# Optimization experiments

Measured on AMD Instinct MI355X. Metric: run time of the kernel, lower is better.

Reference implementation:

```python
import jax, jax.numpy as jnp
import numpy as np

B, S, T, D, H, HD = 1, 2048, 256, 3072, 24, 128
FF = 4 * D
EPS_LN = 1e-6
EPS_RMS = 1e-6


def _layernorm(x):
    m = jnp.mean(x, axis=-1, keepdims=True)
    v = jnp.mean(jnp.square(x - m), axis=-1, keepdims=True)
    return (x - m) * jax.lax.rsqrt(v + EPS_LN)


def _rmsnorm(x, w):
    return x * jax.lax.rsqrt(jnp.mean(jnp.square(x), axis=-1, keepdims=True) + EPS_RMS) * w


def _rope_interleaved(x, cos, sin):
    # x: [B,S,H,HD], cos/sin: [S,HD//2]; non-neox (interleaved) style
    x1 = x[..., 0::2]
    x2 = x[..., 1::2]
    c = cos[None, :, None, :]
    s = sin[None, :, None, :]
    o1 = x1 * c - x2 * s
    o2 = x2 * c + x1 * s
    return jnp.stack([o1, o2], axis=-1).reshape(x.shape)


def setup_inputs() -> dict:
    key = jax.random.key(0)
    ks = jax.random.split(key, 12)

    def n(k, shape, scale):
        return jax.random.normal(k, shape, dtype=jnp.float32) * scale

    # real RoPE tables
    pos = np.arange(S, dtype=np.float64)
    inv_freq = 1.0 / (10000.0 ** (np.arange(0, HD, 2, dtype=np.float64) / HD))
    ang = np.outer(pos, inv_freq)  # [S, HD//2]

    return {
        "img": n(ks[0], (B, S, D), 1.0),
        "vec": n(ks[1], (B, D), 1.0),
        "cos": jnp.asarray(np.cos(ang), jnp.float32),
        "sin": jnp.asarray(np.sin(ang), jnp.float32),
        "k_txt": n(ks[2], (B, T, H, HD), 1.0),
        "v_txt": n(ks[3], (B, T, H, HD), 1.0),
        "mod_w": n(ks[4], (D, 6 * D), 0.02),
        "mod_b": jnp.zeros((6 * D,), jnp.float32),
        "qkv_w": n(ks[5], (D, 3 * D), 0.02),
        "qkv_b": jnp.zeros((3 * D,), jnp.float32),
        "qn_w": jnp.ones((HD,), jnp.float32),
        "kn_w": jnp.ones((HD,), jnp.float32),
        "proj_w": n(ks[6], (D, D), 0.02),
        "proj_b": jnp.zeros((D,), jnp.float32),
        "mlp_w1": n(ks[7], (D, FF), 0.02),
        "mlp_b1": jnp.zeros((FF,), jnp.float32),
        "mlp_w2": n(ks[8], (FF, D), 0.02),
        "mlp_b2": jnp.zeros((D,), jnp.float32),
    }


def reference(img, vec, cos, sin, k_txt, v_txt, mod_w, mod_b, qkv_w, qkv_b,
              qn_w, kn_w, proj_w, proj_b, mlp_w1, mlp_b1, mlp_w2, mlp_b2):
    # modulation: silu(vec) -> linear -> 6 chunks, each [B,1,D]
    mod = jax.nn.silu(vec) @ mod_w + mod_b
    (a_shift, a_scale, a_gate, m_shift, m_scale, m_gate) = [
        m[:, None, :] for m in jnp.split(mod, 6, axis=-1)
    ]

    # LayerNorm (no affine) + scale/shift modulate
    x = _layernorm(img) * (1.0 + a_scale) + a_shift

    qkv = (x @ qkv_w + qkv_b).reshape(B, S, 3, H, HD)
    q, k, v = qkv[:, :, 0], qkv[:, :, 1], qkv[:, :, 2]
    q = _rmsnorm(q, qn_w)
    k = _rmsnorm(k, kn_w)
    q = _rope_interleaved(q, cos, sin)
    k = _rope_interleaved(k, cos, sin)

    # concat text KV cache (no RoPE on text tokens)
    k_all = jnp.concatenate([k, k_txt], axis=1)  # [B,S+T,H,HD]
    v_all = jnp.concatenate([v, v_txt], axis=1)

    scale = 1.0 / jnp.sqrt(jnp.asarray(HD, jnp.float32))
    scores = jnp.einsum('bqhd,bkhd->bhqk', q, k_all) * scale
    probs = jax.nn.softmax(scores, axis=-1)
    attn = jnp.einsum('bhqk,bkhd->bqhd', probs, v_all).reshape(B, S, D)

    attn_out = attn @ proj_w + proj_b

    # ScaleResidualLayerNormScaleShift
    residual = img + a_gate * attn_out
    mlp_in = _layernorm(residual) * (1.0 + m_scale) + m_shift

    mlp_out = jax.nn.gelu(mlp_in @ mlp_w1 + mlp_b1, approximate=True) @ mlp_w2 + mlp_b2
    return residual + m_gate * mlp_out
```

## Files before the change

kernel.cpp:

```cpp
#include <hip/hip_runtime.h>

typedef short short8 __attribute__((ext_vector_type(8)));
typedef float f32x4 __attribute__((ext_vector_type(4)));

#define DEV static __device__ __forceinline__

DEV unsigned short f2bf(float f) {
  union { float f; unsigned u; } v; v.f = f;
  unsigned u = v.u;
  unsigned r = u + 0x7fffu + ((u >> 16) & 1u);
  return (unsigned short)(r >> 16);
}
DEV float bf2f(unsigned short b) {
  union { unsigned u; float f; } v; v.u = ((unsigned)b) << 16;
  return v.f;
}
DEV void load_lds16(const void* g, void* l) {
  __builtin_amdgcn_global_load_lds(
      (const __attribute__((address_space(1))) unsigned int*)g,
      (__attribute__((address_space(3))) unsigned int*)l, 16, 0, 0);
}
DEV int swz(int L) { return L ^ ((L >> 3) & 0x30); }

__global__ __launch_bounds__(256) void zero_mod(const float* __restrict__ b, float* __restrict__ out) {
  int j = blockIdx.x * 256 + threadIdx.x;
  out[j] = b[j];
}

__global__ __launch_bounds__(256) void mod_gemv(const float* __restrict__ vec,
                                                const float* __restrict__ W,
                                                float* __restrict__ out) {
  __shared__ float sv[192];
  int tid = threadIdx.x;
  int kb = blockIdx.y * 192;
  if (tid < 192) {
    float x = vec[kb + tid];
    sv[tid] = x / (1.f + __expf(-x));
  }
  __syncthreads();
  int j = blockIdx.x * 256 + tid;
  float a0 = 0, a1 = 0, a2 = 0, a3 = 0;
  for (int i = 0; i < 192; i += 4) {
    a0 += sv[i + 0] * W[(size_t)(kb + i + 0) * 18432 + j];
    a1 += sv[i + 1] * W[(size_t)(kb + i + 1) * 18432 + j];
    a2 += sv[i + 2] * W[(size_t)(kb + i + 2) * 18432 + j];
    a3 += sv[i + 3] * W[(size_t)(kb + i + 3) * 18432 + j];
  }
  atomicAdd(&out[j], a0 + a1 + a2 + a3);
}

__global__ __launch_bounds__(256) void ln_kernel(const float* __restrict__ in,
                                                 const float* __restrict__ mod,
                                                 int shift_off, int scale_off,
                                                 unsigned short* __restrict__ out) {
  int rowb = blockIdx.x;
  const float* x = in + (size_t)rowb * 3072;
  int tid = threadIdx.x;
  float s = 0.f, ss = 0.f;
  float4 v[3];
#pragma unroll
  for (int r = 0; r < 3; r++) {
    v[r] = *(const float4*)&x[r * 1024 + tid * 4];
    s += v[r].x + v[r].y + v[r].z + v[r].w;
    ss += v[r].x * v[r].x + v[r].y * v[r].y + v[r].z * v[r].z + v[r].w * v[r].w;
  }
#pragma unroll
  for (int m = 32; m; m >>= 1) { s += __shfl_xor(s, m); ss += __shfl_xor(ss, m); }
  __shared__ float red[8];
  int w = tid >> 6, lane = tid & 63;
  if (lane == 0) { red[w] = s; red[4 + w] = ss; }
  __syncthreads();
  s = red[0] + red[1] + red[2] + red[3];
  ss = red[4] + red[5] + red[6] + red[7];
  float mean = s * (1.f / 3072.f);
  float var = ss * (1.f / 3072.f) - mean * mean;
  float rstd = rsqrtf(var + 1e-6f);
#pragma unroll
  for (int r = 0; r < 3; r++) {
    int c = r * 1024 + tid * 4;
    float xv[4] = {v[r].x, v[r].y, v[r].z, v[r].w};
#pragma unroll
    for (int i = 0; i < 4; i++) {
      float o = (xv[i] - mean) * rstd * (1.f + mod[scale_off + c + i]) + mod[shift_off + c + i];
      out[(size_t)rowb * 3072 + c + i] = f2bf(o);
    }
  }
}

__global__ __launch_bounds__(256) void transpose_k(const float* __restrict__ src,
                                                   unsigned short* __restrict__ dst,
                                                   int K, int N) {
  __shared__ float t[64][65];
  int n0 = blockIdx.x * 64, k0 = blockIdx.y * 64;
  int tid = threadIdx.x;
#pragma unroll
  for (int i = 0; i < 16; i++) {
    int lin = i * 256 + tid;
    int r = lin >> 6, c = lin & 63;
    t[r][c] = src[(size_t)(k0 + r) * N + n0 + c];
  }
  __syncthreads();
#pragma unroll
  for (int i = 0; i < 16; i++) {
    int lin = i * 256 + tid;
    int rn = lin >> 6, cn = lin & 63;
    dst[(size_t)(n0 + rn) * K + k0 + cn] = f2bf(t[cn][rn]);
  }
}

__global__ __launch_bounds__(256) void vt_k(const unsigned short* __restrict__ p0,
                                            const unsigned short* __restrict__ p1,
                                            const float* __restrict__ qkv_b,
                                            const float* __restrict__ v_txt,
                                            unsigned short* __restrict__ vt) {
  int h = blockIdx.y;
  int c8 = blockIdx.x * 2 + (threadIdx.x >> 7);
  int d = threadIdx.x & 127;
  int kvb = c8 * 8;
  short8 o;
  if (kvb < 2048) {
    float bias = qkv_b[6144 + h * 128 + d];
#pragma unroll
    for (int j = 0; j < 8; j++) {
      size_t idx = (size_t)(kvb + j) * 9216 + 6144 + h * 128 + d;
      o[j] = (short)f2bf(bf2f(p0[idx]) + bf2f(p1[idx]) + bias);
    }
  } else {
#pragma unroll
    for (int j = 0; j < 8; j++)
      o[j] = (short)f2bf(v_txt[((size_t)(kvb + j - 2048) * 24 + h) * 128 + d]);
  }
  *(short8*)&vt[((size_t)h * 128 + d) * 2304 + kvb] = o;
}

template <int EPI>
__global__ __launch_bounds__(512, 2) void gemm8(const unsigned short* __restrict__ A,
                                                const unsigned short* __restrict__ Bt,
                                                const float* __restrict__ bias,
                                                unsigned short* __restrict__ outb,
                                                int N, int ldk, int klen, size_t zstride) {
  __shared__ unsigned short As[4][8192];
  __shared__ unsigned short Bs[4][8192];
  const int tid = threadIdx.x, lane = tid & 63, w = tid >> 6;
  const int wr = w >> 2, wc = w & 3;
  const int lr = lane & 15, lk = lane >> 4;

  const int bm = blockIdx.y * 256, bn = blockIdx.x * 256;
  const int kbase = blockIdx.z * klen;
  const int NT = klen >> 5;

  const int D0 = tid * 16;
  const int D1 = 8192 + tid * 16;
  const int L0 = swz(D0), L1 = swz(D1);
  const unsigned short* sA0 = A + (size_t)(bm + (L0 >> 6)) * ldk + kbase + ((L0 & 63) >> 1);
  const unsigned short* sA1 = A + (size_t)(bm + (L1 >> 6)) * ldk + kbase + ((L1 & 63) >> 1);
  const unsigned short* sB0 = Bt + (size_t)(bn + (L0 >> 6)) * ldk + kbase + ((L0 & 63) >> 1);
  const unsigned short* sB1 = Bt + (size_t)(bn + (L1 >> 6)) * ldk + kbase + ((L1 & 63) >> 1);

  int aoff[8], boff[4];
#pragma unroll
  for (int mi = 0; mi < 8; mi++)
    aoff[mi] = swz(((wr * 128 + mi * 16 + lr) << 6) | (lk << 4));
#pragma unroll
  for (int ni = 0; ni < 4; ni++)
    boff[ni] = swz(((wc * 64 + ni * 16 + lr) << 6) | (lk << 4));

  f32x4 acc[8][4];
#pragma unroll
  for (int i = 0; i < 8; i++)
#pragma unroll
    for (int j = 0; j < 4; j++) acc[i][j] = (f32x4){0.f, 0.f, 0.f, 0.f};

#pragma unroll
  for (int j = 0; j < 3; j++) {
    load_lds16(sA0 + j * 32, (char*)As + j * 16384 + D0);
    load_lds16(sA1 + j * 32, (char*)As + j * 16384 + D1);
    load_lds16(sB0 + j * 32, (char*)Bs + j * 16384 + D0);
    load_lds16(sB1 + j * 32, (char*)Bs + j * 16384 + D1);
  }
  asm volatile("s_waitcnt vmcnt(8)" ::: "memory");
  __builtin_amdgcn_sched_barrier(0);
  __builtin_amdgcn_s_barrier();

  for (int t = 0; t < NT; ++t) {
    const int rt = t & 3;
    char* Ab = (char*)As + rt * 16384;
    char* Bb = (char*)Bs + rt * 16384;
    const int ss = (t + 3) & 3;
    const int sk = (t + 3) * 32;
    const bool stg = (t + 3) < NT;

    short8 af[8], bf[4];
#pragma unroll
    for (int mi = 0; mi < 8; mi++) af[mi] = *(const short8*)(Ab + aoff[mi]);
#pragma unroll
    for (int ni = 0; ni < 4; ni++) bf[ni] = *(const short8*)(Bb + boff[ni]);
    if (stg) {
      load_lds16(sA0 + sk, (char*)As + ss * 16384 + D0);
      load_lds16(sA1 + sk, (char*)As + ss * 16384 + D1);
      load_lds16(sB0 + sk, (char*)Bs + ss * 16384 + D0);
      load_lds16(sB1 + sk, (char*)Bs + ss * 16384 + D1);
    }
    __builtin_amdgcn_s_setprio(1);
#pragma unroll
    for (int mi = 0; mi < 8; mi++)
#pragma unroll
      for (int ni = 0; ni < 4; ni++)
        acc[mi][ni] = __builtin_amdgcn_mfma_f32_16x16x32_bf16(af[mi], bf[ni], acc[mi][ni], 0, 0, 0);
    __builtin_amdgcn_s_setprio(0);
    if (t < NT - 3) {
      asm volatile("s_waitcnt vmcnt(8)" ::: "memory");
    } else if (t == NT - 3) {
      asm volatile("s_waitcnt vmcnt(4)" ::: "memory");
    } else if (t == NT - 2) {
      asm volatile("s_waitcnt vmcnt(0)" ::: "memory");
    }
    __builtin_amdgcn_sched_barrier(0);
    __builtin_amdgcn_s_barrier();
  }

  const size_t zoff = (size_t)blockIdx.z * zstride;
#pragma unroll
  for (int mi = 0; mi < 8; mi++) {
#pragma unroll
    for (int ni = 0; ni < 4; ni++) {
      int row0 = bm + wr * 128 + mi * 16 + lk * 4;
      int col = bn + wc * 64 + ni * 16 + lr;
#pragma unroll
      for (int r = 0; r < 4; r++) {
        float vv = acc[mi][ni][r];
        if (EPI == 0) {
          outb[(size_t)(row0 + r) * N + col] = f2bf(vv + bias[col]);
        } else if (EPI == 2) {
          float x = vv + bias[col];
          float y = 0.7978845608028654f * (x + 0.044715f * x * x * x);
          float th = 1.f - 2.f / (__expf(2.f * y) + 1.f);
          outb[(size_t)(row0 + r) * N + col] = f2bf(0.5f * x * (1.f + th));
        } else {
          outb[zoff + (size_t)(row0 + r) * N + col] = f2bf(vv);
        }
      }
    }
  }
}

template <int NS>
__global__ __launch_bounds__(256) void sk_epi(const unsigned short* __restrict__ pb,
                                              const float* __restrict__ bias,
                                              const float* __restrict__ addsrc,
                                              const float* __restrict__ gate,
                                              float* __restrict__ out) {
  const int N = 3072;
  const size_t MN = (size_t)2048 * 3072;
  int row = blockIdx.y;
  int col = blockIdx.x * 1024 + threadIdx.x * 4;
  size_t idx = (size_t)row * N + col;
  float4 a = *(const float4*)(addsrc + idx);
  float4 b = *(const float4*)(bias + col);
  float4 g = *(const float4*)(gate + col);
  float sum[4] = {b.x, b.y, b.z, b.w};
#pragma unroll
  for (int s = 0; s < NS; s++) {
    const unsigned short* p = pb + s * MN + idx;
#pragma unroll
    for (int i = 0; i < 4; i++) sum[i] += bf2f(p[i]);
  }
  float4 o;
  o.x = a.x + g.x * sum[0];
  o.y = a.y + g.y * sum[1];
  o.z = a.z + g.z * sum[2];
  o.w = a.w + g.w * sum[3];
  *(float4*)(out + idx) = o;
}

__global__ __launch_bounds__(64) void qkv_post(const unsigned short* __restrict__ p0,
                                               const unsigned short* __restrict__ p1,
                                               const float* __restrict__ qkv_b,
                                               const float* __restrict__ k_txt,
                                               const float* __restrict__ cosb,
                                               const float* __restrict__ sinb,
                                               const float* __restrict__ qn,
                                               const float* __restrict__ kn,
                                               unsigned short* __restrict__ qb,
                                               unsigned short* __restrict__ kb) {
  int s = blockIdx.x, h = blockIdx.y;
  int lane = threadIdx.x;
  int d0 = lane * 2;
  if (s < 2048) {
    size_t rowb = (size_t)s * 9216;
    float c = cosb[s * 64 + lane], sn = sinb[s * 64 + lane];
    const float ascale = 0.08838834764831845f;
    {
      size_t i0 = rowb + h * 128 + d0;
      float a = bf2f(p0[i0]) + bf2f(p1[i0]) + qkv_b[h * 128 + d0];
      float b = bf2f(p0[i0 + 1]) + bf2f(p1[i0 + 1]) + qkv_b[h * 128 + d0 + 1];
      float sq = a * a + b * b;
#pragma unroll
      for (int m = 32; m; m >>= 1) sq += __shfl_xor(sq, m);
      float rr = rsqrtf(sq * (1.f / 128.f) + 1e-6f);
      float x1 = a * rr * qn[d0], x2 = b * rr * qn[d0 + 1];
      float o1 = (x1 * c - x2 * sn) * ascale;
      float o2 = (x2 * c + x1 * sn) * ascale;
      size_t off = ((size_t)h * 2048 + s) * 128 + d0;
      qb[off] = f2bf(o1); qb[off + 1] = f2bf(o2);
    }
    {
      size_t i0 = rowb + 3072 + h * 128 + d0;
      float a = bf2f(p0[i0]) + bf2f(p1[i0]) + qkv_b[3072 + h * 128 + d0];
      float b = bf2f(p0[i0 + 1]) + bf2f(p1[i0 + 1]) + qkv_b[3072 + h * 128 + d0 + 1];
      float sq = a * a + b * b;
#pragma unroll
      for (int m = 32; m; m >>= 1) sq += __shfl_xor(sq, m);
      float rr = rsqrtf(sq * (1.f / 128.f) + 1e-6f);
      float x1 = a * rr * kn[d0], x2 = b * rr * kn[d0 + 1];
      float o1 = x1 * c - x2 * sn;
      float o2 = x2 * c + x1 * sn;
      size_t off = ((size_t)h * 2304 + s) * 128 + d0;
      kb[off] = f2bf(o1); kb[off + 1] = f2bf(o2);
    }
  } else {
    int t = s - 2048;
    size_t src = ((size_t)t * 24 + h) * 128 + d0;
    size_t off = ((size_t)h * 2304 + s) * 128 + d0;
    kb[off] = f2bf(k_txt[src]); kb[off + 1] = f2bf(k_txt[src + 1]);
  }
}

__global__ __launch_bounds__(512) void attn_k(const unsigned short* __restrict__ qb,
                                              const unsigned short* __restrict__ kb,
                                              const unsigned short* __restrict__ vt,
                                              unsigned short* __restrict__ out) {
  __shared__ unsigned short Ks[2][8192];
  __shared__ unsigned short Vs[2][8192];
  __shared__ unsigned short Ps[8][32 * 72];
  int h = blockIdx.y, q0 = blockIdx.x * 256;
  int tid = threadIdx.x, lane = tid & 63, w = tid >> 6;
  int lr = lane & 15, lk = lane >> 4;

  const unsigned short* kh = kb + (size_t)h * 2304 * 128;
  const unsigned short* vth = vt + (size_t)h * 128 * 2304;

  short8 qf[2][4];
#pragma unroll
  for (int mi = 0; mi < 2; mi++)
#pragma unroll
    for (int kf = 0; kf < 4; kf++)
      qf[mi][kf] = *(const short8*)&qb[((size_t)h * 2048 + q0 + w * 32 + mi * 16 + lr) * 128 + kf * 32 + lk * 8];

  const int kR0 = (tid * 16) >> 8, kR1 = (tid * 16 + 8192) >> 8;
  const int kCc = ((tid * 16) >> 4) & 15;
  const int kOf0 = kR0 * 128 + ((kCc ^ (kR0 & 15)) * 8);
  const int kOf1 = kR1 * 128 + ((kCc ^ (kR1 & 15)) * 8);
  const int vR0 = (tid * 16) >> 7, vR1 = (tid * 16 + 8192) >> 7;
  const int vCc = ((tid * 16) >> 4) & 7;
  const int vOf0 = vR0 * 2304 + ((vCc ^ (vR0 & 7)) * 8);
  const int vOf1 = vR1 * 2304 + ((vCc ^ (vR1 & 7)) * 8);

  float mrow[2][4], lsum[2][4];
#pragma unroll
  for (int mi = 0; mi < 2; mi++)
#pragma unroll
    for (int r = 0; r < 4; r++) { mrow[mi][r] = -1e30f; lsum[mi][r] = 0.f; }
  f32x4 oacc[2][8];
#pragma unroll
  for (int mi = 0; mi < 2; mi++)
#pragma unroll
    for (int i = 0; i < 8; i++) oacc[mi][i] = (f32x4){0.f, 0.f, 0.f, 0.f};

  load_lds16(kh + kOf0, (char*)Ks[0] + tid * 16);
  load_lds16(kh + kOf1, (char*)Ks[0] + tid * 16 + 8192);
  load_lds16(vth + vOf0, (char*)Vs[0] + tid * 16);
  load_lds16(vth + vOf1, (char*)Vs[0] + tid * 16 + 8192);
  asm volatile("s_waitcnt vmcnt(0)" ::: "memory");
  __builtin_amdgcn_sched_barrier(0);
  __builtin_amdgcn_s_barrier();

  for (int kt = 0; kt < 36; kt++) {
    const int cur = kt & 1, nxt = cur ^ 1;
    if (kt + 1 < 36) {
      int kv1 = (kt + 1) * 64;
      load_lds16(kh + (size_t)kv1 * 128 + kOf0, (char*)Ks[nxt] + tid * 16);
      load_lds16(kh + (size_t)kv1 * 128 + kOf1, (char*)Ks[nxt] + tid * 16 + 8192);
      load_lds16(vth + kv1 + vOf0, (char*)Vs[nxt] + tid * 16);
      load_lds16(vth + kv1 + vOf1, (char*)Vs[nxt] + tid * 16 + 8192);
    }

    f32x4 sa[2][4];
#pragma unroll
    for (int mi = 0; mi < 2; mi++)
#pragma unroll
      for (int ni = 0; ni < 4; ni++) sa[mi][ni] = (f32x4){0.f, 0.f, 0.f, 0.f};
    __builtin_amdgcn_s_setprio(1);
#pragma unroll
    for (int kf = 0; kf < 4; kf++) {
#pragma unroll
      for (int ni = 0; ni < 4; ni++) {
        int n = ni * 16 + lr;
        short8 bfr = *(const short8*)&Ks[cur][n * 128 + (((kf * 4 + lk) ^ lr) & 15) * 8];
        sa[0][ni] = __builtin_amdgcn_mfma_f32_16x16x32_bf16(qf[0][kf], bfr, sa[0][ni], 0, 0, 0);
        sa[1][ni] = __builtin_amdgcn_mfma_f32_16x16x32_bf16(qf[1][kf], bfr, sa[1][ni], 0, 0, 0);
      }
    }
    __builtin_amdgcn_s_setprio(0);

#pragma unroll
    for (int mi = 0; mi < 2; mi++) {
#pragma unroll
      for (int r = 0; r < 4; r++) {
        float mx = fmaxf(fmaxf(sa[mi][0][r], sa[mi][1][r]), fmaxf(sa[mi][2][r], sa[mi][3][r]));
#pragma unroll
        for (int m = 8; m; m >>= 1) mx = fmaxf(mx, __shfl_xor(mx, m));
        float mnew = fmaxf(mrow[mi][r], mx);
        float p0 = __expf(sa[mi][0][r] - mnew);
        float p1 = __expf(sa[mi][1][r] - mnew);
        float p2 = __expf(sa[mi][2][r] - mnew);
        float p3 = __expf(sa[mi][3][r] - mnew);
        float su = p0 + p1 + p2 + p3;
#pragma unroll
        for (int m = 8; m; m >>= 1) su += __shfl_xor(su, m);
        float alpha = __expf(mrow[mi][r] - mnew);
        lsum[mi][r] = lsum[mi][r] * alpha + su;
        mrow[mi][r] = mnew;
#pragma unroll
        for (int df = 0; df < 8; df++) oacc[mi][df][r] *= alpha;
        int prow = (mi * 16 + lk * 4 + r) * 72;
        Ps[w][prow + 0 * 16 + lr] = f2bf(p0);
        Ps[w][prow + 1 * 16 + lr] = f2bf(p1);
        Ps[w][prow + 2 * 16 + lr] = f2bf(p2);
        Ps[w][prow + 3 * 16 + lr] = f2bf(p3);
      }
    }

    __builtin_amdgcn_s_setprio(1);
#pragma unroll
    for (int kf2 = 0; kf2 < 2; kf2++) {
      short8 pa0 = *(const short8*)&Ps[w][(0 * 16 + lr) * 72 + kf2 * 32 + lk * 8];
      short8 pa1 = *(const short8*)&Ps[w][(1 * 16 + lr) * 72 + kf2 * 32 + lk * 8];
#pragma unroll
      for (int df = 0; df < 8; df++) {
        int d = df * 16 + lr;
        short8 bv = *(const short8*)&Vs[cur][d * 64 + (((kf2 * 4 + lk) ^ (lr & 7)) & 7) * 8];
        oacc[0][df] = __builtin_amdgcn_mfma_f32_16x16x32_bf16(pa0, bv, oacc[0][df], 0, 0, 0);
        oacc[1][df] = __builtin_amdgcn_mfma_f32_16x16x32_bf16(pa1, bv, oacc[1][df], 0, 0, 0);
      }
    }
    __builtin_amdgcn_s_setprio(0);

    asm volatile("s_waitcnt vmcnt(0)" ::: "memory");
    __builtin_amdgcn_sched_barrier(0);
    __builtin_amdgcn_s_barrier();
  }

#pragma unroll
  for (int mi = 0; mi < 2; mi++) {
#pragma unroll
    for (int r = 0; r < 4; r++) {
      float inv = 1.f / lsum[mi][r];
      int row = q0 + w * 32 + mi * 16 + lk * 4 + r;
#pragma unroll
      for (int df = 0; df < 8; df++)
        out[(size_t)row * 3072 + h * 128 + df * 16 + lr] = f2bf(oacc[mi][df][r] * inv);
    }
  }
}

extern "C" void kernel_launch(void* const* d_in, const int* in_sizes, int n_in,
                              void* d_out, int out_size, void* d_ws, size_t ws_size,
                              hipStream_t stream) {
  const float* img = (const float*)d_in[0];
  const float* vec = (const float*)d_in[1];
  const float* cosb = (const float*)d_in[2];
  const float* sinb = (const float*)d_in[3];
  const float* k_txt = (const float*)d_in[4];
  const float* v_txt = (const float*)d_in[5];
  const float* mod_w = (const float*)d_in[6];
  const float* mod_b = (const float*)d_in[7];
  const float* qkv_w = (const float*)d_in[8];
  const float* qkv_b = (const float*)d_in[9];
  const float* qn_w = (const float*)d_in[10];
  const float* kn_w = (const float*)d_in[11];
  const float* proj_w = (const float*)d_in[12];
  const float* proj_b = (const float*)d_in[13];
  const float* mlp_w1 = (const float*)d_in[14];
  const float* mlp_b1 = (const float*)d_in[15];
  const float* mlp_w2 = (const float*)d_in[16];
  const float* mlp_b2 = (const float*)d_in[17];
  float* outp = (float*)d_out;

  const size_t MN = (size_t)2048 * 3072;
  char* ws = (char*)d_ws;
  unsigned short* qbuf = (unsigned short*)(ws + 0);
  unsigned short* kbuf = (unsigned short*)(ws + 12582912);
  unsigned short* vtbuf = (unsigned short*)(ws + 26738688);
  unsigned short* qp0 = (unsigned short*)(ws + 40894464);
  unsigned short* qp1 = (unsigned short*)(ws + 78643200);
  const size_t qzstride = (78643200 - 40894464) / 2;
  unsigned short* pbuf = (unsigned short*)(ws + 50331648);
  unsigned short* attnb = (unsigned short*)(ws + 78643200);
  float* resid = (float*)(ws + 91226112);
  unsigned short* xln = (unsigned short*)(ws + 116391936);
  float* modv = (float*)(ws + 128974848);
  unsigned short* wt = (unsigned short*)(ws + 129048576);
  unsigned short* hbuf = (unsigned short*)(ws + 0);

  zero_mod<<<72, 256, 0, stream>>>(mod_b, modv);
  mod_gemv<<<dim3(72, 16), 256, 0, stream>>>(vec, mod_w, modv);

  ln_kernel<<<2048, 256, 0, stream>>>(img, modv, 0, 3072, xln);

  transpose_k<<<dim3(144, 48), 256, 0, stream>>>(qkv_w, wt, 3072, 9216);
  gemm8<3><<<dim3(36, 8, 2), 512, 0, stream>>>(xln, wt, nullptr, qp0, 9216, 3072, 1536, qzstride);

  qkv_post<<<dim3(2304, 24), 64, 0, stream>>>(qp0, qp1, qkv_b, k_txt, cosb, sinb,
                                              qn_w, kn_w, qbuf, kbuf);
  vt_k<<<dim3(144, 24), 256, 0, stream>>>(qp0, qp1, qkv_b, v_txt, vtbuf);

  attn_k<<<dim3(8, 24), 512, 0, stream>>>(qbuf, kbuf, vtbuf, attnb);

  transpose_k<<<dim3(48, 48), 256, 0, stream>>>(proj_w, wt, 3072, 3072);
  gemm8<3><<<dim3(12, 8, 2), 512, 0, stream>>>(attnb, wt, nullptr, pbuf, 3072, 3072, 1536, MN);
  sk_epi<2><<<dim3(3, 2048), 256, 0, stream>>>(pbuf, proj_b, img, modv + 2 * 3072, resid);

  ln_kernel<<<2048, 256, 0, stream>>>(resid, modv, 3 * 3072, 4 * 3072, xln);

  transpose_k<<<dim3(192, 48), 256, 0, stream>>>(mlp_w1, wt, 3072, 12288);
  gemm8<2><<<dim3(48, 8, 1), 512, 0, stream>>>(xln, wt, mlp_b1, hbuf, 12288, 3072, 3072, 0);

  transpose_k<<<dim3(48, 192), 256, 0, stream>>>(mlp_w2, wt, 12288, 3072);
  gemm8<3><<<dim3(12, 8, 2), 512, 0, stream>>>(hbuf, wt, nullptr, pbuf, 3072, 12288, 6144, MN);
  sk_epi<2><<<dim3(3, 2048), 256, 0, stream>>>(pbuf, mlp_b2, resid, modv + 5 * 3072, outp);
}
```

Measured before the change: 939.0 us.

## Halve attention block size and single-buffer V with split K/V pipeline

```diff
diff --git a/kernel.cpp b/kernel.cpp
--- a/kernel.cpp
+++ b/kernel.cpp
@@ -326,14 +326,14 @@
   }
 }
 
-__global__ __launch_bounds__(512) void attn_k(const unsigned short* __restrict__ qb,
+__global__ __launch_bounds__(256) void attn_k(const unsigned short* __restrict__ qb,
                                               const unsigned short* __restrict__ kb,
                                               const unsigned short* __restrict__ vt,
                                               unsigned short* __restrict__ out) {
   __shared__ unsigned short Ks[2][8192];
-  __shared__ unsigned short Vs[2][8192];
-  __shared__ unsigned short Ps[8][32 * 72];
-  int h = blockIdx.y, q0 = blockIdx.x * 256;
+  __shared__ unsigned short Vs[8192];
+  __shared__ unsigned short Ps[4][32 * 72];
+  int h = blockIdx.y, q0 = blockIdx.x * 128;
   int tid = threadIdx.x, lane = tid & 63, w = tid >> 6;
   int lr = lane & 15, lk = lane >> 4;
 
@@ -347,14 +347,16 @@
     for (int kf = 0; kf < 4; kf++)
       qf[mi][kf] = *(const short8*)&qb[((size_t)h * 2048 + q0 + w * 32 + mi * 16 + lr) * 128 + kf * 32 + lk * 8];
 
-  const int kR0 = (tid * 16) >> 8, kR1 = (tid * 16 + 8192) >> 8;
-  const int kCc = ((tid * 16) >> 4) & 15;
-  const int kOf0 = kR0 * 128 + ((kCc ^ (kR0 & 15)) * 8);
-  const int kOf1 = kR1 * 128 + ((kCc ^ (kR1 & 15)) * 8);
-  const int vR0 = (tid * 16) >> 7, vR1 = (tid * 16 + 8192) >> 7;
-  const int vCc = ((tid * 16) >> 4) & 7;
-  const int vOf0 = vR0 * 2304 + ((vCc ^ (vR0 & 7)) * 8);
-  const int vOf1 = vR1 * 2304 + ((vCc ^ (vR1 & 7)) * 8);
+  int kOf[4], vOf[4], dOf[4];
+#pragma unroll
+  for (int i = 0; i < 4; i++) {
+    int o = i * 4096 + tid * 16;
+    dOf[i] = o;
+    int kR = o >> 8, kC = (o >> 4) & 15;
+    kOf[i] = kR * 128 + ((kC ^ (kR & 15)) * 8);
+    int vR = o >> 7, vC = (o >> 4) & 7;
+    vOf[i] = vR * 2304 + ((vC ^ (vR & 7)) * 8);
+  }
 
   float mrow[2][4], lsum[2][4];
 #pragma unroll
@@ -367,22 +369,22 @@
 #pragma unroll
     for (int i = 0; i < 8; i++) oacc[mi][i] = (f32x4){0.f, 0.f, 0.f, 0.f};
 
-  load_lds16(kh + kOf0, (char*)Ks[0] + tid * 16);
-  load_lds16(kh + kOf1, (char*)Ks[0] + tid * 16 + 8192);
-  load_lds16(vth + vOf0, (char*)Vs[0] + tid * 16);
-  load_lds16(vth + vOf1, (char*)Vs[0] + tid * 16 + 8192);
+#pragma unroll
+  for (int i = 0; i < 4; i++) load_lds16(vth + vOf[i], (char*)Vs + dOf[i]);
+#pragma unroll
+  for (int i = 0; i < 4; i++) load_lds16(kh + kOf[i], (char*)Ks[0] + dOf[i]);
   asm volatile("s_waitcnt vmcnt(0)" ::: "memory");
   __builtin_amdgcn_sched_barrier(0);
   __builtin_amdgcn_s_barrier();
 
   for (int kt = 0; kt < 36; kt++) {
-    const int cur = kt & 1, nxt = cur ^ 1;
-    if (kt + 1 < 36) {
-      int kv1 = (kt + 1) * 64;
-      load_lds16(kh + (size_t)kv1 * 128 + kOf0, (char*)Ks[nxt] + tid * 16);
-      load_lds16(kh + (size_t)kv1 * 128 + kOf1, (char*)Ks[nxt] + tid * 16 + 8192);
-      load_lds16(vth + kv1 + vOf0, (char*)Vs[nxt] + tid * 16);
-      load_lds16(vth + kv1 + vOf1, (char*)Vs[nxt] + tid * 16 + 8192);
+    const int cur = kt & 1;
+    const bool more = (kt + 1 < 36);
+    if (more) {
+      size_t kb1 = (size_t)(kt + 1) * 64 * 128;
+#pragma unroll
+      for (int i = 0; i < 4; i++)
+        load_lds16(kh + kb1 + kOf[i], (char*)Ks[cur ^ 1] + dOf[i]);
     }
 
     f32x4 sa[2][4];
@@ -431,6 +433,14 @@
       }
     }
 
+    if (more) {
+      asm volatile("s_waitcnt vmcnt(4)" ::: "memory");
+    } else {
+      asm volatile("s_waitcnt vmcnt(0)" ::: "memory");
+    }
+    __builtin_amdgcn_sched_barrier(0);
+    __builtin_amdgcn_s_barrier();
+
     __builtin_amdgcn_s_setprio(1);
 #pragma unroll
     for (int kf2 = 0; kf2 < 2; kf2++) {
@@ -439,16 +449,23 @@
 #pragma unroll
       for (int df = 0; df < 8; df++) {
         int d = df * 16 + lr;
-        short8 bv = *(const short8*)&Vs[cur][d * 64 + (((kf2 * 4 + lk) ^ (lr & 7)) & 7) * 8];
+        short8 bv = *(const short8*)&Vs[d * 64 + (((kf2 * 4 + lk) ^ (lr & 7)) & 7) * 8];
         oacc[0][df] = __builtin_amdgcn_mfma_f32_16x16x32_bf16(pa0, bv, oacc[0][df], 0, 0, 0);
         oacc[1][df] = __builtin_amdgcn_mfma_f32_16x16x32_bf16(pa1, bv, oacc[1][df], 0, 0, 0);
       }
     }
     __builtin_amdgcn_s_setprio(0);
 
-    asm volatile("s_waitcnt vmcnt(0)" ::: "memory");
-    __builtin_amdgcn_sched_barrier(0);
-    __builtin_amdgcn_s_barrier();
+    if (more) {
+      __builtin_amdgcn_s_barrier();
+      size_t vb1 = (size_t)(kt + 1) * 64;
+#pragma unroll
+      for (int i = 0; i < 4; i++)
+        load_lds16(vth + vb1 + vOf[i], (char*)Vs + dOf[i]);
+      asm volatile("s_waitcnt vmcnt(4)" ::: "memory");
+      __builtin_amdgcn_sched_barrier(0);
+      __builtin_amdgcn_s_barrier();
+    }
   }
 
 #pragma unroll
@@ -515,7 +532,7 @@
                                               qn_w, kn_w, qbuf, kbuf);
   vt_k<<<dim3(144, 24), 256, 0, stream>>>(qp0, qp1, qkv_b, v_txt, vtbuf);
 
-  attn_k<<<dim3(8, 24), 512, 0, stream>>>(qbuf, kbuf, vtbuf, attnb);
+  attn_k<<<dim3(16, 24), 256, 0, stream>>>(qbuf, kbuf, vtbuf, attnb);
 
   transpose_k<<<dim3(48, 48), 256, 0, stream>>>(proj_w, wt, 3072, 3072);
   gemm8<3><<<dim3(12, 8, 2), 512, 0, stream>>>(attnb, wt, nullptr, pbuf, 3072, 3072, 1536, MN);
```

After: 947.5 us. Within noise of the previous version (+0.9%).
